# Optimization experiments

Hardware: AMD Instinct MI355X
Metric: run time of the kernel (lower is better)

## Reference

```python
import jax, jax.numpy as jnp
import numpy as np

B, C, Fd, T = 128, 3, 128, 1000
FM, TM, NF, NT = 12, 15, 2, 2   # freq_mask, time_mask, n_freq, n_time
NOISE_STD = 0.04


def setup_inputs() -> dict:
    key = jax.random.key(0)
    ks = jax.random.split(key, 6)
    x = jax.random.normal(ks[0], (B, C, Fd, T), dtype=jnp.float32)
    noise = jax.random.normal(ks[1], (B, C, Fd, T), dtype=jnp.float32)
    # mask lengths: torch.randint(1, max(2, min(fm, F)))
    f_len = jax.random.randint(ks[2], (B, NF), 1, max(2, min(FM, Fd)), dtype=jnp.int32)
    t_len = jax.random.randint(ks[3], (B, NT), 1, max(2, min(TM, T)), dtype=jnp.int32)
    # mask starts: torch.randint(0, max(1, F - f)) — data-dependent upper bound,
    # realized via uniform * (F - len)
    f0 = (jax.random.uniform(ks[4], (B, NF)) * (Fd - f_len)).astype(jnp.int32)
    t0 = (jax.random.uniform(ks[5], (B, NT)) * (T - t_len)).astype(jnp.int32)
    return {"x": x, "noise": noise, "f0": f0, "f_len": f_len, "t0": t0, "t_len": t_len}


def reference(x, noise, f0, f_len, t0, t_len):
    # x: [B, C, F, T]; additive gaussian noise then per-sample freq/time zero masks
    x = x + noise * NOISE_STD
    fi = jnp.arange(x.shape[2])[None, None, :]                       # [1,1,F]
    fmask = jnp.any((fi >= f0[:, :, None]) & (fi < (f0 + f_len)[:, :, None]), axis=1)  # [B,F]
    ti = jnp.arange(x.shape[3])[None, None, :]                       # [1,1,T]
    tmask = jnp.any((ti >= t0[:, :, None]) & (ti < (t0 + t_len)[:, :, None]), axis=1)  # [B,T]
    keep = (~fmask)[:, None, :, None] & (~tmask)[:, None, None, :]   # [B,1,F,T]
    return x * keep
```

## Files before the change

kernel.cpp:

```cpp
#include <hip/hip_runtime.h>
#include <hip/hip_bf16.h>


#define B 128
#define C 3
#define Fd 128
#define T 1000
#define NOISE_STD 0.04f

__global__ __launch_bounds__(256) void specaug_kernel(
    const float* __restrict__ x, const float* __restrict__ noise,
    const int* __restrict__ f0, const int* __restrict__ f_len,
    const int* __restrict__ t0, const int* __restrict__ t_len,
    float* __restrict__ out)
{
    const int row = blockIdx.x;
    const int f   = row % Fd;
    const int b   = row / (C * Fd);
    const int tid = threadIdx.x;

    const int fa0 = f0[b * 2 + 0], fl0 = f_len[b * 2 + 0];
    const int fa1 = f0[b * 2 + 1], fl1 = f_len[b * 2 + 1];
    const bool fmask = (f >= fa0 && f < fa0 + fl0) || (f >= fa1 && f < fa1 + fl1);

    const long long base = (long long)row * T;

    if (tid >= 250) return;

    float4* outp = reinterpret_cast<float4*>(out + base) + tid;

    if (fmask) {
        float4 z; z.x = 0.f; z.y = 0.f; z.z = 0.f; z.w = 0.f;
        *outp = z;
        return;
    }

    const int ta0 = t0[b * 2 + 0], tl0 = t_len[b * 2 + 0];
    const int ta1 = t0[b * 2 + 1], tl1 = t_len[b * 2 + 1];

    const float4 xv = *(reinterpret_cast<const float4*>(x + base) + tid);
    const float4 nv = *(reinterpret_cast<const float4*>(noise + base) + tid);

    const int t = tid * 4;
    float r[4];
    const float xs[4] = {xv.x, xv.y, xv.z, xv.w};
    const float ns[4] = {nv.x, nv.y, nv.z, nv.w};
#pragma unroll
    for (int k = 0; k < 4; ++k) {
        const int tt = t + k;
        const bool tmask = (tt >= ta0 && tt < ta0 + tl0) || (tt >= ta1 && tt < ta1 + tl1);
        r[k] = tmask ? 0.f : fmaf(ns[k], NOISE_STD, xs[k]);
    }
    float4 ov; ov.x = r[0]; ov.y = r[1]; ov.z = r[2]; ov.w = r[3];
    *outp = ov;
}

extern "C" void kernel_launch(void* const* d_in, const int* in_sizes, int n_in,
                              void* d_out, int out_size, void* d_ws, size_t ws_size,
                              hipStream_t stream)
{
    const float* x     = (const float*)d_in[0];
    const float* noise = (const float*)d_in[1];
    const int*   f0    = (const int*)d_in[2];
    const int*   f_len = (const int*)d_in[3];
    const int*   t0    = (const int*)d_in[4];
    const int*   t_len = (const int*)d_in[5];
    float* out = (float*)d_out;

    const int nrows = B * C * Fd;
    specaug_kernel<<<nrows, 256, 0, stream>>>(x, noise, f0, f_len, t0, t_len, out);
}
```

Measured before the change: 102.7 us.

## Use flat grid-stride loop with nontemporal stores over float4 elements

Replaces the one-block-per-row launch, which left 6 of 256 threads idle in every block, with a fixed 2048-block grid-stride loop over a flat index of float4 elements. Outputs are written with nontemporal stores to limit cache pollution, and the per-sample mask parameters are read as int2 vector loads. The change adds an integer divide and reloads of the mask parameters on every loop iteration. It also depends on the fixed grid size giving enough memory-level parallelism.

```diff
diff --git a/kernel.cpp b/kernel.cpp
--- a/kernel.cpp
+++ b/kernel.cpp
@@ -8,51 +8,58 @@
 #define T 1000
 #define NOISE_STD 0.04f
 
+typedef float  f32x4 __attribute__((ext_vector_type(4)));
+typedef int    i32x2 __attribute__((ext_vector_type(2)));
+
+constexpr int ROWS       = B * C * Fd;
+constexpr int V4_PER_ROW = T / 4;
+constexpr int NV4        = ROWS * V4_PER_ROW;
+
 __global__ __launch_bounds__(256) void specaug_kernel(
     const float* __restrict__ x, const float* __restrict__ noise,
     const int* __restrict__ f0, const int* __restrict__ f_len,
     const int* __restrict__ t0, const int* __restrict__ t_len,
     float* __restrict__ out)
 {
-    const int row = blockIdx.x;
-    const int f   = row % Fd;
-    const int b   = row / (C * Fd);
-    const int tid = threadIdx.x;
+    const int gid    = blockIdx.x * blockDim.x + threadIdx.x;
+    const int stride = gridDim.x * blockDim.x;
 
-    const int fa0 = f0[b * 2 + 0], fl0 = f_len[b * 2 + 0];
-    const int fa1 = f0[b * 2 + 1], fl1 = f_len[b * 2 + 1];
-    const bool fmask = (f >= fa0 && f < fa0 + fl0) || (f >= fa1 && f < fa1 + fl1);
+    for (int i = gid; i < NV4; i += stride) {
+        const unsigned row = (unsigned)i / (unsigned)V4_PER_ROW;
+        const int rem = i - (int)row * V4_PER_ROW;
+        const int b   = (int)(row / (unsigned)(C * Fd));
+        const int f   = (int)(row & (Fd - 1));
 
-    const long long base = (long long)row * T;
+        const i32x2 fa = reinterpret_cast<const i32x2*>(f0)[b];
+        const i32x2 fl = reinterpret_cast<const i32x2*>(f_len)[b];
+        const bool fmask = (f >= fa.x && f < fa.x + fl.x) ||
+                           (f >= fa.y && f < fa.y + fl.y);
 
-    if (tid >= 250) return;
+        f32x4* outp = reinterpret_cast<f32x4*>(out) + i;
 
-    float4* outp = reinterpret_cast<float4*>(out + base) + tid;
+        if (fmask) {
+            f32x4 z = {0.f, 0.f, 0.f, 0.f};
+            __builtin_nontemporal_store(z, outp);
+            continue;
+        }
 
-    if (fmask) {
-        float4 z; z.x = 0.f; z.y = 0.f; z.z = 0.f; z.w = 0.f;
-        *outp = z;
-        return;
+        const i32x2 ta = reinterpret_cast<const i32x2*>(t0)[b];
+        const i32x2 tl = reinterpret_cast<const i32x2*>(t_len)[b];
+
+        const f32x4 xv = reinterpret_cast<const f32x4*>(x)[i];
+        const f32x4 nv = reinterpret_cast<const f32x4*>(noise)[i];
+
+        const int t = rem * 4;
+        f32x4 ov;
+#pragma unroll
+        for (int k = 0; k < 4; ++k) {
+            const int tt = t + k;
+            const bool tmask = (tt >= ta.x && tt < ta.x + tl.x) ||
+                               (tt >= ta.y && tt < ta.y + tl.y);
+            ov[k] = tmask ? 0.f : fmaf(nv[k], NOISE_STD, xv[k]);
+        }
+        __builtin_nontemporal_store(ov, outp);
     }
-
-    const int ta0 = t0[b * 2 + 0], tl0 = t_len[b * 2 + 0];
-    const int ta1 = t0[b * 2 + 1], tl1 = t_len[b * 2 + 1];
-
-    const float4 xv = *(reinterpret_cast<const float4*>(x + base) + tid);
-    const float4 nv = *(reinterpret_cast<const float4*>(noise + base) + tid);
-
-    const int t = tid * 4;
-    float r[4];
-    const float xs[4] = {xv.x, xv.y, xv.z, xv.w};
-    const float ns[4] = {nv.x, nv.y, nv.z, nv.w};
-#pragma unroll
-    for (int k = 0; k < 4; ++k) {
-        const int tt = t + k;
-        const bool tmask = (tt >= ta0 && tt < ta0 + tl0) || (tt >= ta1 && tt < ta1 + tl1);
-        r[k] = tmask ? 0.f : fmaf(ns[k], NOISE_STD, xs[k]);
-    }
-    float4 ov; ov.x = r[0]; ov.y = r[1]; ov.z = r[2]; ov.w = r[3];
-    *outp = ov;
 }
 
 extern "C" void kernel_launch(void* const* d_in, const int* in_sizes, int n_in,
@@ -67,6 +74,6 @@
     const int*   t_len = (const int*)d_in[5];
     float* out = (float*)d_out;
 
-    const int nrows = B * C * Fd;
-    specaug_kernel<<<nrows, 256, 0, stream>>>(x, noise, f0, f_len, t0, t_len, out);
+    const int nblocks = 2048;
+    specaug_kernel<<<nblocks, 256, 0, stream>>>(x, noise, f0, f_len, t0, t_len, out);
 }
```

New measurement: 115.9 us. 12.8% more time.
